# Kernel tuning notes

Hardware: AMD Instinct MI355X
Metric: run time of the kernel (lower is better)

The kernel has to match this reference:

```python
import jax, jax.numpy as jnp
import numpy as np

DEGREE = 3
N_BASIS = 16


def _clamped_knots(n_basis, degree):
    # Clamped uniform knot vector on [0, 1]: degree+1 repeated knots at each end.
    n_interior = n_basis - degree - 1
    interior = np.linspace(0.0, 1.0, n_interior + 2)[1:-1]
    knots = np.concatenate([np.zeros(degree + 1), interior, np.ones(degree + 1)])
    return jnp.asarray(knots, dtype=jnp.float32)


def bspline_basis(x, degree=DEGREE, n_basis=N_BASIS):
    # Cox-de Boor recursion, vectorized over all leading dims of x.
    # x: (...,) in [0,1] -> (..., n_basis)
    t = _clamped_knots(n_basis, degree)
    n_knots = n_basis + degree + 1
    xe = jnp.clip(x, 0.0, 1.0 - 1e-6)[..., None]
    B = ((xe >= t[:-1]) & (xe < t[1:])).astype(x.dtype)  # (..., n_knots-1)
    for p in range(1, degree + 1):
        dl = t[p:n_knots - 1] - t[:n_knots - 1 - p]
        dr = t[p + 1:n_knots] - t[1:n_knots - p]
        left = jnp.where(dl > 0, (xe - t[:n_knots - 1 - p]) / jnp.where(dl > 0, dl, 1.0), 0.0)
        right = jnp.where(dr > 0, (t[p + 1:n_knots] - xe) / jnp.where(dr > 0, dr, 1.0), 0.0)
        B = left * B[..., :-1] + right * B[..., 1:]
    return B  # (..., n_basis)


def _kl(cm, lv):
    # KL(N(cm, exp(lv)) || N(0, 1)) summed over all edges/coeffs (prior_scale = 1).
    var = jnp.exp(lv)
    return 0.5 * jnp.sum(var + cm * cm - 1.0 - lv)


def _layer(x, cm, lv):
    # x: (B, in); cm, lv: (out, in, n_basis)
    basis = bspline_basis(x)  # (B, in, n_basis)
    out = jnp.einsum('bik,oik->bo', basis, cm)  # fused per-edge weighted sum
    return out, _kl(cm, lv)


def setup_inputs() -> dict:
    key = jax.random.key(0)
    ks = jax.random.split(key, 4)
    B = 8192
    sizes = [256, 512, 512, 256]
    nb = N_BASIS
    inp = {"x": jax.random.uniform(ks[0], (B, sizes[0]), dtype=jnp.float32)}
    for i in range(3):
        inp[f"cm{i}"] = 0.1 * jax.random.normal(ks[1 + i], (sizes[i + 1], sizes[i], nb), dtype=jnp.float32)
        inp[f"lv{i}"] = -2.0 * jnp.ones((sizes[i + 1], sizes[i], nb), dtype=jnp.float32)
    return inp


def reference(x, cm0, lv0, cm1, lv1, cm2, lv2):
    out = x
    kl = jnp.zeros((), x.dtype)
    for cm, lv in ((cm0, lv0), (cm1, lv1), (cm2, lv2)):
        out, k = _layer(out, cm, lv)
        kl = kl + k
    return out, kl
```

## Files before the change

### kernel.cpp

```cpp
#include <hip/hip_runtime.h>
#include <hip/hip_bf16.h>


typedef __attribute__((ext_vector_type(8))) _Float16 f16x8;
typedef __attribute__((ext_vector_type(4))) float float4v;
typedef unsigned short ushort_t;

__device__ __forceinline__ ushort_t f2h(float f) {
  _Float16 h = (_Float16)f;
  return *(ushort_t*)&h;
}
__device__ __forceinline__ float h2f(ushort_t u) {
  return (float)*(_Float16*)&u;
}

__device__ __forceinline__ void bspline_w4(float x, int& k0, float w[4]) {
  const float XMAX = 1.0f - 1e-6f;
  float xe = fminf(fmaxf(x, 0.0f), XMAX);
  int cell = (int)(xe * 13.0f);
  cell = cell > 12 ? 12 : cell;
  k0 = cell;
  int j = cell + 3;
  const float s = 1.0f / 13.0f;
  int cjm2 = max(j - 5, 0);
  int cjm1 = max(j - 4, 0);
  int cj   = j - 3;
  int cj1  = j - 2;
  int cj2  = min(j - 1, 13);
  int cj3  = min(j, 13);
  float tjm1 = cjm1 * s, tj = cj * s;
  float tjm2 = cjm2 * s;
  float tj1 = cj1 * s, tj2 = cj2 * s, tj3 = cj3 * s;
  float left1 = xe - tj, left2 = xe - tjm1, left3 = xe - tjm2;
  float right1 = tj1 - xe, right2 = tj2 - xe, right3 = tj3 - xe;
#define INV3(d) ((d) == 1 ? 13.0f : ((d) == 2 ? 6.5f : (13.0f / 3.0f)))
  float i10 = INV3(cj1 - cj);
  float i20 = INV3(cj1 - cjm1), i21 = INV3(cj2 - cj);
  float i30 = INV3(cj1 - cjm2), i31 = INV3(cj2 - cjm1), i32 = INV3(cj3 - cj);
#undef INV3
  float temp = i10;
  float N0 = right1 * temp;
  float N1 = left1 * temp;
  temp = N0 * i20;
  N0 = right1 * temp;
  float saved = left2 * temp;
  temp = N1 * i21;
  N1 = saved + right2 * temp;
  float N2 = left1 * temp;
  temp = N0 * i30;
  N0 = right1 * temp;
  saved = left3 * temp;
  temp = N1 * i31;
  N1 = saved + right2 * temp;
  saved = left2 * temp;
  temp = N2 * i32;
  N2 = saved + right3 * temp;
  float N3 = left1 * temp;
  w[0] = N0; w[1] = N1; w[2] = N2; w[3] = N3;
}

template <bool SPLIT_A>
__global__ __launch_bounds__(256, 3) void kan_layer(
    const float* __restrict__ act, const ushort_t* __restrict__ Bsw,
    float* __restrict__ outp, int IN, int OUT) {
  const int K = IN * 16;
  const int KC = K >> 3;
  __shared__ ushort_t Ah[2][128 * 72];
  __shared__ ushort_t Al[SPLIT_A ? 2 : 1][SPLIT_A ? 128 * 72 : 1];

  const int tid = threadIdx.x;
  const int lane = tid & 63;
  const int wv = tid >> 6;
  const int wm = wv >> 1, wn = wv & 1;
  const int quad = lane >> 4, l15 = lane & 15;
  const int b0 = blockIdx.x * 128;
  const int n0 = blockIdx.y * 128;
  const int tbase = (n0 >> 4) + wn * 4;

  float4v acc[4][4];
#pragma unroll
  for (int a = 0; a < 4; a++)
#pragma unroll
    for (int b = 0; b < 4; b++) acc[a][b] = (float4v)0.0f;

  const int gm = tid >> 1;
  const int gip = (tid & 1) * 2;
  const float* xrow = &act[(size_t)(b0 + gm) * IN + gip];

  const ushort_t* bbase[4];
#pragma unroll
  for (int nt = 0; nt < 4; ++nt)
    bbase[nt] = Bsw + (size_t)(tbase + nt) * KC * 128 + lane * 8;

  const int nsteps = K / 64;
  const int chunk = nsteps / gridDim.z;
  const int kbeg = blockIdx.z * chunk;
  const int kend = kbeg + chunk;
  const int klast = kend - 1;

#define EVAL_WRITE(BUF, XV)                                                   \
  {                                                                           \
    int k0a, k0b; float wa[4], wb[4];                                         \
    bspline_w4((XV).x, k0a, wa);                                              \
    bspline_w4((XV).y, k0b, wb);                                              \
    uint4 z4; z4.x = z4.y = z4.z = z4.w = 0u;                                 \
    ushort_t* arow_h = &Ah[BUF][gm * 72 + gip * 16];                          \
    ((uint4*)arow_h)[0] = z4; ((uint4*)arow_h)[1] = z4;                       \
    ((uint4*)arow_h)[2] = z4; ((uint4*)arow_h)[3] = z4;                       \
    _Pragma("unroll")                                                         \
    for (int t = 0; t < 4; ++t) {                                             \
      arow_h[k0a + t] = f2h(wa[t]);                                           \
      arow_h[16 + k0b + t] = f2h(wb[t]);                                      \
    }                                                                         \
    if (SPLIT_A) {                                                            \
      ushort_t* arow_l = &Al[BUF][gm * 72 + gip * 16];                        \
      ((uint4*)arow_l)[0] = z4; ((uint4*)arow_l)[1] = z4;                     \
      ((uint4*)arow_l)[2] = z4; ((uint4*)arow_l)[3] = z4;                     \
      _Pragma("unroll")                                                       \
      for (int t = 0; t < 4; ++t) {                                           \
        arow_l[k0a + t] = f2h(wa[t] - h2f(f2h(wa[t])));                       \
        arow_l[16 + k0b + t] = f2h(wb[t] - h2f(f2h(wb[t])));                  \
      }                                                                       \
    }                                                                         \
  }

#define MFMA_STEP(BUF, BF)                                                    \
  _Pragma("unroll")                                                           \
  for (int ks = 0; ks < 2; ++ks) {                                            \
    f16x8 ahf[4], alf[4];                                                     \
    _Pragma("unroll")                                                         \
    for (int mt = 0; mt < 4; ++mt) {                                          \
      int off = (wm * 64 + mt * 16 + l15) * 72 + ks * 32 + quad * 8;          \
      ahf[mt] = *(const f16x8*)&Ah[BUF][off];                                 \
      if (SPLIT_A) alf[mt] = *(const f16x8*)&Al[BUF][off];                    \
    }                                                                         \
    _Pragma("unroll")                                                         \
    for (int mt = 0; mt < 4; ++mt)                                            \
      _Pragma("unroll")                                                       \
      for (int nt = 0; nt < 4; ++nt) {                                        \
        if (SPLIT_A)                                                          \
          acc[mt][nt] = __builtin_amdgcn_mfma_f32_16x16x32_f16(               \
              alf[mt], (BF)[ks][nt], acc[mt][nt], 0, 0, 0);                   \
        acc[mt][nt] = __builtin_amdgcn_mfma_f32_16x16x32_f16(                 \
            ahf[mt], (BF)[ks][nt], acc[mt][nt], 0, 0, 0);                     \
      }                                                                       \
  }

#define KSTEP_BODY(KS, CUR, BFC, BFN, XVC, XVN)                               \
  {                                                                           \
    const int kp1 = ((KS) + 1 <= klast) ? (KS) + 1 : klast;                   \
    const int kp2 = ((KS) + 2 <= klast) ? (KS) + 2 : klast;                   \
    _Pragma("unroll")                                                         \
    for (int ks = 0; ks < 2; ++ks)                                            \
      _Pragma("unroll")                                                       \
      for (int nt = 0; nt < 4; ++nt)                                          \
        BFN[ks][nt] =                                                         \
            *(const f16x8*)&bbase[nt][(size_t)kp1 * 1024 + ks * 512];         \
    XVN = *(const float2*)&xrow[kp2 * 4];                                     \
    MFMA_STEP(CUR, BFC);                                                      \
    EVAL_WRITE((CUR) ^ 1, XVC);                                               \
    __syncthreads();                                                          \
  }

  f16x8 bf0[2][4], bf1[2][4];
#pragma unroll
  for (int ks = 0; ks < 2; ++ks)
#pragma unroll
    for (int nt = 0; nt < 4; ++nt)
      bf0[ks][nt] = *(const f16x8*)&bbase[nt][(size_t)kbeg * 1024 + ks * 512];
  float2 xvP = *(const float2*)&xrow[kbeg * 4];
  float2 xv0 = *(const float2*)&xrow[((kbeg + 1 <= klast) ? kbeg + 1 : klast) * 4];
  float2 xv1;
  EVAL_WRITE(0, xvP);
  __syncthreads();

  for (int k = kbeg; k < kend; k += 2) {
    KSTEP_BODY(k,     0, bf0, bf1, xv0, xv1);
    KSTEP_BODY(k + 1, 1, bf1, bf0, xv1, xv0);
  }

#undef KSTEP_BODY
#undef MFMA_STEP
#undef EVAL_WRITE

#pragma unroll
  for (int mt = 0; mt < 4; ++mt)
#pragma unroll
    for (int nt = 0; nt < 4; ++nt) {
      int col = n0 + wn * 64 + nt * 16 + l15;
#pragma unroll
      for (int r = 0; r < 4; ++r) {
        int row = b0 + wm * 64 + mt * 16 + quad * 4 + r;
        atomicAdd(&outp[(size_t)row * OUT + col], acc[mt][nt][r]);
      }
    }
}

__global__ __launch_bounds__(256) void kl_convert(
    const float* __restrict__ cm, const float* __restrict__ lv,
    ushort_t* __restrict__ bsw, int G ,
    long long ngroups, float* __restrict__ klout) {
  long long i = (long long)blockIdx.x * blockDim.x + threadIdx.x;
  const long long stride = (long long)gridDim.x * blockDim.x;
  float s = 0.0f;
  for (; i < ngroups; i += stride) {
    int o = (int)(i / G);
    int kc = (int)(i - (long long)o * G);
    const float* cp = &cm[i * 8];
    const float* lp = &lv[i * 8];
    unsigned pk[4];
#pragma unroll
    for (int t = 0; t < 4; ++t) {
      float c0 = cp[2 * t], c1 = cp[2 * t + 1];
      float l0 = lp[2 * t], l1 = lp[2 * t + 1];
      pk[t] = (unsigned)f2h(c0) | ((unsigned)f2h(c1) << 16);
      s += 0.5f * (__expf(l0) + c0 * c0 - 1.0f - l0);
      s += 0.5f * (__expf(l1) + c1 * c1 - 1.0f - l1);
    }
    uint4 v; v.x = pk[0]; v.y = pk[1]; v.z = pk[2]; v.w = pk[3];
    size_t doff = (((size_t)(o >> 4) * G + kc) * 16 + (o & 15)) * 8;
    *(uint4*)&bsw[doff] = v;
  }
#pragma unroll
  for (int off = 32; off > 0; off >>= 1) s += __shfl_down(s, off, 64);
  __shared__ float red[4];
  int wv = threadIdx.x >> 6;
  if ((threadIdx.x & 63) == 0) red[wv] = s;
  __syncthreads();
  if (threadIdx.x == 0)
    atomicAdd(klout, red[0] + red[1] + red[2] + red[3]);
}

extern "C" void kernel_launch(void* const* d_in, const int* in_sizes, int n_in,
                              void* d_out, int out_size, void* d_ws, size_t ws_size,
                              hipStream_t stream) {
  const float* x   = (const float*)d_in[0];
  const float* cm0 = (const float*)d_in[1];
  const float* lv0 = (const float*)d_in[2];
  const float* cm1 = (const float*)d_in[3];
  const float* lv1 = (const float*)d_in[4];
  const float* cm2 = (const float*)d_in[5];
  const float* lv2 = (const float*)d_in[6];

  float* out = (float*)d_out;
  float* klp = out + (size_t)8192 * 256;

  char* ws = (char*)d_ws;
  float*    act1 = (float*)(ws);
  float*    act2 = (float*)(ws + ((size_t)16 << 20));
  ushort_t* b0sw = (ushort_t*)(ws + ((size_t)32 << 20));
  ushort_t* b1sw = (ushort_t*)(ws + ((size_t)36 << 20));
  ushort_t* b2sw = (ushort_t*)(ws + ((size_t)44 << 20));

  hipMemsetAsync(ws, 0, (size_t)32 << 20, stream);
  hipMemsetAsync(d_out, 0, (size_t)out_size * sizeof(float), stream);

  kl_convert<<<2048, 256, 0, stream>>>(cm0, lv0, b0sw, 256 * 2, 512LL * 256 * 2, klp);
  kl_convert<<<2048, 256, 0, stream>>>(cm1, lv1, b1sw, 512 * 2, 512LL * 512 * 2, klp);
  kl_convert<<<2048, 256, 0, stream>>>(cm2, lv2, b2sw, 512 * 2, 256LL * 512 * 2, klp);

  kan_layer<true ><<<dim3(64, 4, 4), 256, 0, stream>>>(x,    b0sw, act1, 256, 512);
  kan_layer<false><<<dim3(64, 4, 4), 256, 0, stream>>>(act1, b1sw, act2, 512, 512);
  kan_layer<false><<<dim3(64, 2, 8), 256, 0, stream>>>(act2, b2sw, out,  512, 256);
}
```

Before: 517.3 us.

## Shrink block tile to 64 rows with four waves splitting N

Changes the per-block tile from 128x128 (2x2 waves, 4x4 MFMA tiles each) to 64x128 with four waves each covering 32 columns, halving per-wave accumulators and B fragments. Each thread now evaluates one B-spline input instead of two, and the grid doubles in x. The aim is lower register and LDS use so more blocks fit per CU (launch bound raised to 4) and more blocks overall. The cost is that every weight tile is loaded from global memory by twice as many blocks, and the MFMA work per synchronisation drops.

```diff
diff --git a/kernel.cpp b/kernel.cpp
--- a/kernel.cpp
+++ b/kernel.cpp
@@ -60,36 +60,35 @@
 }
 
 template <bool SPLIT_A>
-__global__ __launch_bounds__(256, 3) void kan_layer(
+__global__ __launch_bounds__(256, 4) void kan_layer(
     const float* __restrict__ act, const ushort_t* __restrict__ Bsw,
     float* __restrict__ outp, int IN, int OUT) {
   const int K = IN * 16;
   const int KC = K >> 3;
-  __shared__ ushort_t Ah[2][128 * 72];
-  __shared__ ushort_t Al[SPLIT_A ? 2 : 1][SPLIT_A ? 128 * 72 : 1];
+  __shared__ ushort_t Ah[2][64 * 72];
+  __shared__ ushort_t Al[SPLIT_A ? 2 : 1][SPLIT_A ? 64 * 72 : 1];
 
   const int tid = threadIdx.x;
   const int lane = tid & 63;
-  const int wv = tid >> 6;
-  const int wm = wv >> 1, wn = wv & 1;
+  const int wn = tid >> 6;
   const int quad = lane >> 4, l15 = lane & 15;
-  const int b0 = blockIdx.x * 128;
+  const int b0 = blockIdx.x * 64;
   const int n0 = blockIdx.y * 128;
-  const int tbase = (n0 >> 4) + wn * 4;
-
-  float4v acc[4][4];
+  const int tbase = (n0 >> 4) + wn * 2;
+
+  float4v acc[4][2];
 #pragma unroll
   for (int a = 0; a < 4; a++)
 #pragma unroll
-    for (int b = 0; b < 4; b++) acc[a][b] = (float4v)0.0f;
-
-  const int gm = tid >> 1;
-  const int gip = (tid & 1) * 2;
-  const float* xrow = &act[(size_t)(b0 + gm) * IN + gip];
-
-  const ushort_t* bbase[4];
-#pragma unroll
-  for (int nt = 0; nt < 4; ++nt)
+    for (int b = 0; b < 2; b++) acc[a][b] = (float4v)0.0f;
+
+  const int gm = tid >> 2;
+  const int gf = tid & 3;
+  const float* xrow = &act[(size_t)(b0 + gm) * IN + gf];
+
+  const ushort_t* bbase[2];
+#pragma unroll
+  for (int nt = 0; nt < 2; ++nt)
     bbase[nt] = Bsw + (size_t)(tbase + nt) * KC * 128 + lane * 8;
 
   const int nsteps = K / 64;
@@ -98,29 +97,21 @@
   const int kend = kbeg + chunk;
   const int klast = kend - 1;
 
-#define EVAL_WRITE(BUF, XV)                                                   \
+#define EVAL_WRITE(BUF, XS)                                                   \
   {                                                                           \
-    int k0a, k0b; float wa[4], wb[4];                                         \
-    bspline_w4((XV).x, k0a, wa);                                              \
-    bspline_w4((XV).y, k0b, wb);                                              \
+    int k0a; float wa[4];                                                     \
+    bspline_w4(XS, k0a, wa);                                                  \
     uint4 z4; z4.x = z4.y = z4.z = z4.w = 0u;                                 \
-    ushort_t* arow_h = &Ah[BUF][gm * 72 + gip * 16];                          \
+    ushort_t* arow_h = &Ah[BUF][gm * 72 + gf * 16];                           \
     ((uint4*)arow_h)[0] = z4; ((uint4*)arow_h)[1] = z4;                       \
-    ((uint4*)arow_h)[2] = z4; ((uint4*)arow_h)[3] = z4;                       \
-    _Pragma("unroll")                                                         \
-    for (int t = 0; t < 4; ++t) {                                             \
-      arow_h[k0a + t] = f2h(wa[t]);                                           \
-      arow_h[16 + k0b + t] = f2h(wb[t]);                                      \
-    }                                                                         \
+    _Pragma("unroll")                                                         \
+    for (int t = 0; t < 4; ++t) arow_h[k0a + t] = f2h(wa[t]);                 \
     if (SPLIT_A) {                                                            \
-      ushort_t* arow_l = &Al[BUF][gm * 72 + gip * 16];                        \
+      ushort_t* arow_l = &Al[BUF][gm * 72 + gf * 16];                         \
       ((uint4*)arow_l)[0] = z4; ((uint4*)arow_l)[1] = z4;                     \
-      ((uint4*)arow_l)[2] = z4; ((uint4*)arow_l)[3] = z4;                     \
       _Pragma("unroll")                                                       \
-      for (int t = 0; t < 4; ++t) {                                           \
+      for (int t = 0; t < 4; ++t)                                             \
         arow_l[k0a + t] = f2h(wa[t] - h2f(f2h(wa[t])));                       \
-        arow_l[16 + k0b + t] = f2h(wb[t] - h2f(f2h(wb[t])));                  \
-      }                                                                       \
     }                                                                         \
   }
 
@@ -130,14 +121,14 @@
     f16x8 ahf[4], alf[4];                                                     \
     _Pragma("unroll")                                                         \
     for (int mt = 0; mt < 4; ++mt) {                                          \
-      int off = (wm * 64 + mt * 16 + l15) * 72 + ks * 32 + quad * 8;          \
+      int off = (mt * 16 + l15) * 72 + ks * 32 + quad * 8;                    \
       ahf[mt] = *(const f16x8*)&Ah[BUF][off];                                 \
       if (SPLIT_A) alf[mt] = *(const f16x8*)&Al[BUF][off];                    \
     }                                                                         \
     _Pragma("unroll")                                                         \
     for (int mt = 0; mt < 4; ++mt)                                            \
       _Pragma("unroll")                                                       \
-      for (int nt = 0; nt < 4; ++nt) {                                        \
+      for (int nt = 0; nt < 2; ++nt) {                                        \
         if (SPLIT_A)                                                          \
           acc[mt][nt] = __builtin_amdgcn_mfma_f32_16x16x32_f16(               \
               alf[mt], (BF)[ks][nt], acc[mt][nt], 0, 0, 0);                   \
@@ -153,24 +144,24 @@
     _Pragma("unroll")                                                         \
     for (int ks = 0; ks < 2; ++ks)                                            \
       _Pragma("unroll")                                                       \
-      for (int nt = 0; nt < 4; ++nt)                                          \
+      for (int nt = 0; nt < 2; ++nt)                                          \
         BFN[ks][nt] =                                                         \
             *(const f16x8*)&bbase[nt][(size_t)kp1 * 1024 + ks * 512];         \
-    XVN = *(const float2*)&xrow[kp2 * 4];                                     \
+    XVN = xrow[kp2 * 4];                                                      \
     MFMA_STEP(CUR, BFC);                                                      \
     EVAL_WRITE((CUR) ^ 1, XVC);                                               \
     __syncthreads();                                                          \
   }
 
-  f16x8 bf0[2][4], bf1[2][4];
+  f16x8 bf0[2][2], bf1[2][2];
 #pragma unroll
   for (int ks = 0; ks < 2; ++ks)
 #pragma unroll
-    for (int nt = 0; nt < 4; ++nt)
+    for (int nt = 0; nt < 2; ++nt)
       bf0[ks][nt] = *(const f16x8*)&bbase[nt][(size_t)kbeg * 1024 + ks * 512];
-  float2 xvP = *(const float2*)&xrow[kbeg * 4];
-  float2 xv0 = *(const float2*)&xrow[((kbeg + 1 <= klast) ? kbeg + 1 : klast) * 4];
-  float2 xv1;
+  float xvP = xrow[kbeg * 4];
+  float xv0 = xrow[((kbeg + 1 <= klast) ? kbeg + 1 : klast) * 4];
+  float xv1;
   EVAL_WRITE(0, xvP);
   __syncthreads();
 
@@ -186,11 +177,11 @@
 #pragma unroll
   for (int mt = 0; mt < 4; ++mt)
 #pragma unroll
-    for (int nt = 0; nt < 4; ++nt) {
-      int col = n0 + wn * 64 + nt * 16 + l15;
+    for (int nt = 0; nt < 2; ++nt) {
+      int col = n0 + wn * 32 + nt * 16 + l15;
 #pragma unroll
       for (int r = 0; r < 4; ++r) {
-        int row = b0 + wm * 64 + mt * 16 + quad * 4 + r;
+        int row = b0 + mt * 16 + quad * 4 + r;
         atomicAdd(&outp[(size_t)row * OUT + col], acc[mt][nt][r]);
       }
     }
@@ -259,7 +250,7 @@
   kl_convert<<<2048, 256, 0, stream>>>(cm1, lv1, b1sw, 512 * 2, 512LL * 512 * 2, klp);
   kl_convert<<<2048, 256, 0, stream>>>(cm2, lv2, b2sw, 512 * 2, 256LL * 512 * 2, klp);
 
-  kan_layer<true ><<<dim3(64, 4, 4), 256, 0, stream>>>(x,    b0sw, act1, 256, 512);
-  kan_layer<false><<<dim3(64, 4, 4), 256, 0, stream>>>(act1, b1sw, act2, 512, 512);
-  kan_layer<false><<<dim3(64, 2, 8), 256, 0, stream>>>(act2, b2sw, out,  512, 256);
-}
+  kan_layer<true ><<<dim3(128, 4, 4), 256, 0, stream>>>(x,    b0sw, act1, 256, 512);
+  kan_layer<false><<<dim3(128, 4, 4), 256, 0, stream>>>(act1, b1sw, act2, 512, 512);
+  kan_layer<false><<<dim3(128, 2, 8), 256, 0, stream>>>(act2, b2sw, out,  512, 256);
+}
```

Result: faster. 461.5 us (-10.8%).
